# Optimization experiments

Hardware: AMD Instinct MI355X
Metric: run time of the kernel (lower is better)

Reference implementation:

```python
import jax, jax.numpy as jnp
import numpy as np

B, S, HID = 4, 1024, 1024
NH, HD = 16, 64  # num_heads, head_size
LEFT, RIGHT = 64, 8
NUM_POS = LEFT + RIGHT + 1  # 73


def setup_inputs() -> dict:
    key = jax.random.key(0)
    ks = jax.random.split(key, 11)
    s = 0.02
    return {
        "hidden_states": jax.random.normal(ks[0], (B, S, HID), jnp.float32),
        "Wq": jax.random.normal(ks[1], (HID, HID), jnp.float32) * s,
        "bq": jax.random.normal(ks[2], (HID,), jnp.float32) * s,
        "Wk": jax.random.normal(ks[3], (HID, HID), jnp.float32) * s,
        "bk": jax.random.normal(ks[4], (HID,), jnp.float32) * s,
        "Wv": jax.random.normal(ks[5], (HID, HID), jnp.float32) * s,
        "bv": jax.random.normal(ks[6], (HID,), jnp.float32) * s,
        "Wo": jax.random.normal(ks[7], (HID, HID), jnp.float32) * s,
        "bo": jax.random.normal(ks[8], (HID,), jnp.float32) * s,
        "dist_emb": jax.random.normal(ks[9], (NUM_POS, HD), jnp.float32) * s,
    }


def reference(hidden_states, Wq, bq, Wk, bk, Wv, bv, Wo, bo, dist_emb):
    inv_sqrt_d = 1.0 / np.sqrt(HD).astype(np.float32)
    # projections; nn.Linear: x @ W.T + b
    q = (hidden_states @ Wq.T + bq).reshape(B, S, NH, HD).transpose(0, 2, 1, 3)  # bhld
    k = (hidden_states @ Wk.T + bk).reshape(B, S, NH, HD).transpose(0, 2, 1, 3)
    v = (hidden_states @ Wv.T + bv).reshape(B, S, NH, HD).transpose(0, 2, 1, 3)

    scores = jnp.einsum("bhld,bhrd->bhlr", q, k) * inv_sqrt_d

    # relative_key bias
    pos_l = jnp.arange(S)[:, None]
    pos_r = jnp.arange(S)[None, :]
    dist = jnp.clip(pos_r - pos_l, -LEFT, RIGHT) + LEFT  # [S,S] in [0, NUM_POS)
    pos_emb = dist_emb[dist]  # [S,S,HD]
    rel = jnp.einsum("bhld,lrd->bhlr", q, pos_emb) * inv_sqrt_d
    scores = scores + rel

    probs = jax.nn.softmax(scores, axis=-1)  # dropout p=0 (eval)
    ctx = jnp.einsum("bhlr,bhrd->bhld", probs, v)
    ctx = ctx.transpose(0, 2, 1, 3).reshape(B, S, HID)
    out = ctx @ Wo.T + bo
    return (out, probs)
```

## Files before the change

### kernel.cpp

```cpp
#include <hip/hip_runtime.h>


using short8 = __attribute__((ext_vector_type(8))) short;
using f32x4  = __attribute__((ext_vector_type(4))) float;
using fl4    = __attribute__((ext_vector_type(4))) float;
using u16x4  = __attribute__((ext_vector_type(4))) unsigned short;

#define MFMA16(a, b, c) __builtin_amdgcn_mfma_f32_16x16x32_bf16((a), (b), (c), 0, 0, 0)

#define SCL2E 0.18033688011112042f

__device__ __forceinline__ float bf2f(unsigned short u) {
  union { unsigned int i; float f; } c;
  c.i = ((unsigned int)u) << 16;
  return c.f;
}
__device__ __forceinline__ unsigned short f2bf(float f) {
  union { float f; unsigned int i; } c;
  c.f = f;
  unsigned int x = c.i;
  return (unsigned short)((x + 0x7fffu + ((x >> 16) & 1u)) >> 16);
}
__device__ __forceinline__ float u2f(unsigned u) {
  union { unsigned i; float f; } c;
  c.i = u;
  return c.f;
}

__device__ __forceinline__ void gload_lds16(const void* g, void* l) {
  __builtin_amdgcn_global_load_lds(
      (const __attribute__((address_space(1))) void*)g,
      (__attribute__((address_space(3))) void*)l, 16, 0, 0);
}

__global__ void cvt_f32_bf16(const float* __restrict__ in,
                             unsigned short* __restrict__ out, int n4) {
  int i = blockIdx.x * blockDim.x + threadIdx.x;
  int stride = gridDim.x * blockDim.x;
  for (; i < n4; i += stride) {
    fl4 v = ((const fl4*)in)[i];
    u16x4 o;
    o[0] = f2bf(v[0]); o[1] = f2bf(v[1]); o[2] = f2bf(v[2]); o[3] = f2bf(v[3]);
    ((u16x4*)out)[i] = o;
  }
}

__global__ void cvt_w4(const float* __restrict__ w0, const float* __restrict__ w1,
                       const float* __restrict__ w2, const float* __restrict__ w3,
                       unsigned short* __restrict__ o0, unsigned short* __restrict__ o1,
                       unsigned short* __restrict__ o2, unsigned short* __restrict__ o3) {
  const int which = blockIdx.x >> 8;
  const float* in = which == 0 ? w0 : which == 1 ? w1 : which == 2 ? w2 : w3;
  unsigned short* out = which == 0 ? o0 : which == 1 ? o1 : which == 2 ? o2 : o3;
  int i = (blockIdx.x & 255) * 256 + threadIdx.x;
#pragma unroll
  for (int it = 0; it < 4; ++it, i += 65536) {
    fl4 v = ((const fl4*)in)[i];
    u16x4 o;
    o[0] = f2bf(v[0]); o[1] = f2bf(v[1]); o[2] = f2bf(v[2]); o[3] = f2bf(v[3]);
    ((u16x4*)out)[i] = o;
  }
}

__global__ void cvt_demb(const float* __restrict__ in,
                         unsigned short* __restrict__ out) {
  int i = blockIdx.x * blockDim.x + threadIdx.x;
  if (i < 80 * 64) out[i] = (i < 73 * 64) ? f2bf(in[i]) : (unsigned short)0;
}

__global__ __launch_bounds__(256)
void gemm_qkv3(const unsigned short* __restrict__ X,
               const unsigned short* __restrict__ Bq,
               const unsigned short* __restrict__ Bk,
               const unsigned short* __restrict__ Bv,
               const float* __restrict__ biq, const float* __restrict__ bik,
               const float* __restrict__ biv,
               unsigned short* __restrict__ Cq, unsigned short* __restrict__ Ck,
               unsigned short* __restrict__ Cvt) {
  __shared__ unsigned short lA[128 * 32];
  __shared__ unsigned short lB[128 * 32];
  const int i = blockIdx.x;
  const int wgid = (i & 7) * 96 + (i >> 3);
  const int r = wgid >> 8;
  const int id = wgid & 255;
  int bm, bn;
  const unsigned short *Aa, *Bb;
  if (r == 2) {
    bm = (id >> 5) * 128; bn = (id & 31) * 128;
    Aa = Bv; Bb = X;
  } else {
    bm = (id >> 3) * 128; bn = (id & 7) * 128;
    Aa = X; Bb = (r == 0) ? Bq : Bk;
  }
  const float* bias = (r == 0) ? biq : (r == 1) ? bik : biv;
  unsigned short* C = (r == 0) ? Cq : (r == 1) ? Ck : Cvt;
  const size_t cstride = (r == 2) ? 4096 : 1024;

  const int tid = threadIdx.x;
  const int wave = tid >> 6, lane = tid & 63;
  const int wm = wave >> 1, wn = wave & 1;

  f32x4 acc[4][4];
#pragma unroll
  for (int m = 0; m < 4; ++m)
#pragma unroll
    for (int n = 0; n < 4; ++n) acc[m][n] = (f32x4){0.f, 0.f, 0.f, 0.f};

  const int t0 = tid, t1 = tid + 256;
  const int ar0 = t0 >> 2, ak0 = (t0 & 3) * 8;
  const int ar1 = t1 >> 2, ak1 = (t1 & 3) * 8;
  const unsigned short* Ab = Aa + (size_t)bm * 1024;
  const unsigned short* Bbb = Bb + (size_t)bn * 1024;
  const int fr = lane & 15, fk = (lane >> 4) * 8;

  for (int kt = 0; kt < 1024; kt += 32) {
    gload_lds16(Ab + (size_t)ar0 * 1024 + kt + ak0, (void*)&lA[(wave * 64) * 8]);
    gload_lds16(Ab + (size_t)ar1 * 1024 + kt + ak1, (void*)&lA[2048 + (wave * 64) * 8]);
    gload_lds16(Bbb + (size_t)ar0 * 1024 + kt + ak0, (void*)&lB[(wave * 64) * 8]);
    gload_lds16(Bbb + (size_t)ar1 * 1024 + kt + ak1, (void*)&lB[2048 + (wave * 64) * 8]);
    __syncthreads();
    short8 af[4], bf[4];
#pragma unroll
    for (int m = 0; m < 4; ++m)
      af[m] = *(const short8*)&lA[(wm * 64 + m * 16 + fr) * 32 + fk];
#pragma unroll
    for (int n = 0; n < 4; ++n)
      bf[n] = *(const short8*)&lB[(wn * 64 + n * 16 + fr) * 32 + fk];
#pragma unroll
    for (int m = 0; m < 4; ++m)
#pragma unroll
      for (int n = 0; n < 4; ++n) acc[m][n] = MFMA16(af[m], bf[n], acc[m][n]);
    __syncthreads();
  }

  const int cr = (lane >> 4) * 4, cc = lane & 15;
#pragma unroll
  for (int m = 0; m < 4; ++m)
#pragma unroll
    for (int n = 0; n < 4; ++n) {
      const int col = bn + wn * 64 + n * 16 + cc;
#pragma unroll
      for (int g = 0; g < 4; ++g) {
        const int row = bm + wm * 64 + m * 16 + cr + g;
        const float bb = (r == 2) ? bias[row] : bias[col];
        C[(size_t)row * cstride + col] = f2bf(acc[m][n][g] + bb);
      }
    }
}

__global__ __launch_bounds__(256)
void gemm_nt_f32(const unsigned short* __restrict__ A,
                 const unsigned short* __restrict__ B,
                 const float* __restrict__ bias, float* __restrict__ Cp) {
  __shared__ unsigned short lA[128 * 32];
  __shared__ unsigned short lB[128 * 32];
  const int tid = threadIdx.x;
  const int wave = tid >> 6, lane = tid & 63;
  const int wm = wave >> 1, wn = wave & 1;
  const int bm = blockIdx.x * 128, bn = blockIdx.y * 128;

  f32x4 acc[4][4];
#pragma unroll
  for (int m = 0; m < 4; ++m)
#pragma unroll
    for (int n = 0; n < 4; ++n) acc[m][n] = (f32x4){0.f, 0.f, 0.f, 0.f};

  const int t0 = tid, t1 = tid + 256;
  const int ar0 = t0 >> 2, ak0 = (t0 & 3) * 8;
  const int ar1 = t1 >> 2, ak1 = (t1 & 3) * 8;
  const unsigned short* Ab = A + (size_t)bm * 1024;
  const unsigned short* Bb = B + (size_t)bn * 1024;
  const int fr = lane & 15, fk = (lane >> 4) * 8;

  for (int kt = 0; kt < 1024; kt += 32) {
    gload_lds16(Ab + (size_t)ar0 * 1024 + kt + ak0, (void*)&lA[(wave * 64) * 8]);
    gload_lds16(Ab + (size_t)ar1 * 1024 + kt + ak1, (void*)&lA[2048 + (wave * 64) * 8]);
    gload_lds16(Bb + (size_t)ar0 * 1024 + kt + ak0, (void*)&lB[(wave * 64) * 8]);
    gload_lds16(Bb + (size_t)ar1 * 1024 + kt + ak1, (void*)&lB[2048 + (wave * 64) * 8]);
    __syncthreads();
    short8 af[4], bf[4];
#pragma unroll
    for (int m = 0; m < 4; ++m)
      af[m] = *(const short8*)&lA[(wm * 64 + m * 16 + fr) * 32 + fk];
#pragma unroll
    for (int n = 0; n < 4; ++n)
      bf[n] = *(const short8*)&lB[(wn * 64 + n * 16 + fr) * 32 + fk];
#pragma unroll
    for (int m = 0; m < 4; ++m)
#pragma unroll
      for (int n = 0; n < 4; ++n) acc[m][n] = MFMA16(af[m], bf[n], acc[m][n]);
    __syncthreads();
  }

  const int cr = (lane >> 4) * 4, cc = lane & 15;
#pragma unroll
  for (int m = 0; m < 4; ++m)
#pragma unroll
    for (int n = 0; n < 4; ++n) {
      const int col = bn + wn * 64 + n * 16 + cc;
#pragma unroll
      for (int g = 0; g < 4; ++g) {
        const int row = bm + wm * 64 + m * 16 + cr + g;
        Cp[(size_t)row * 1024 + col] = acc[m][n][g] + bias[col];
      }
    }
}

__global__ __launch_bounds__(256, 2)
void attn_kernel(const unsigned short* __restrict__ q,
                 const unsigned short* __restrict__ k,
                 const unsigned short* __restrict__ vt,
                 const unsigned short* __restrict__ demb_bf,
                 float* __restrict__ probs,
                 unsigned short* __restrict__ ctx) {
  const int i = blockIdx.x;
  const int x = i & 7, s = i >> 3;
  const int bh = ((s >> 5) << 3) + x;
  const int qseg = s & 31;
  const int hd = bh & 15, b = bh >> 4;
  const int tid = threadIdx.x, w = tid >> 6, lane = tid & 63;
  const int lq = lane & 15, Qr = lane >> 4;
  const int qA = qseg * 32, qB = qA + 16;
  const int rowperm = ((lq >> 2) << 3) + (lq & 3);

  __shared__ unsigned short qdc[32][78];
  __shared__ float reds[4][32];
  __shared__ float red[4][4][32][16];

  const unsigned short* qpA =
      q + ((size_t)(b * 1024 + qA + lq)) * 1024 + hd * 64 + Qr * 8;
  short8 bqA0 = *(const short8*)qpA;
  short8 bqA1 = *(const short8*)(qpA + 32);
  const unsigned short* qpB = qpA + (size_t)16 * 1024;
  short8 bqB0 = *(const short8*)qpB;
  short8 bqB1 = *(const short8*)(qpB + 32);

  for (int pgq = w; pgq < 10; pgq += 4) {
    const int qblk = pgq >= 5;
    const int pg = qblk ? pgq - 5 : pgq;
    const unsigned short* dp = demb_bf + (size_t)(pg * 16 + lq) * 64 + Qr * 8;
    short8 a0 = *(const short8*)dp;
    short8 a1 = *(const short8*)(dp + 32);
    f32x4 c = (f32x4){0.f, 0.f, 0.f, 0.f};
    c = MFMA16(a0, qblk ? bqB0 : bqA0, c);
    c = MFMA16(a1, qblk ? bqB1 : bqA1, c);
#pragma unroll
    for (int g = 0; g < 4; ++g) {
      const int p = pg * 16 + Qr * 4 + g;
      if (p < 73) qdc[qblk * 16 + lq][p] = f2bf(c[g] * SCL2E);
    }
  }
  __syncthreads();

  const float qd0A = bf2f(qdc[lq][0]),       qd72A = bf2f(qdc[lq][72]);
  const float qd0B = bf2f(qdc[16 + lq][0]),  qd72B = bf2f(qdc[16 + lq][72]);

  float ssumA = 0.f, ssumB = 0.f;
  unsigned pafA[8][4], pafB[8][4];
  f32x4 oA0 = (f32x4){0.f, 0.f, 0.f, 0.f}, oA1 = oA0, oA2 = oA0, oA3 = oA0;
  f32x4 oB0 = oA0, oB1 = oA0, oB2 = oA0, oB3 = oA0;
  const unsigned short* kbase =
      k + ((size_t)(b * 1024 + w * 256 + rowperm)) * 1024 + hd * 64 + Qr * 8;
  const unsigned short* vb =
      vt + ((size_t)(hd * 64 + lq)) * 4096 + b * 1024 + w * 256 + Qr * 8;

#pragma unroll
  for (int t = 0; t < 8; ++t) {
    const unsigned short* kp = kbase + t * 32768;
    short8 ae0 = *(const short8*)kp;
    short8 ae1 = *(const short8*)(kp + 32);
    short8 ao0 = *(const short8*)(kp + 4096);
    short8 ao1 = *(const short8*)(kp + 4128);
    short8 v0 = *(const short8*)(vb + t * 32);
    short8 v1 = *(const short8*)(vb + (size_t)16 * 4096 + t * 32);
    short8 v2 = *(const short8*)(vb + (size_t)32 * 4096 + t * 32);
    short8 v3 = *(const short8*)(vb + (size_t)48 * 4096 + t * 32);

    f32x4 seA = (f32x4){0.f, 0.f, 0.f, 0.f}, soA = seA, seB = seA, soB = seA;
    seA = MFMA16(ae0, bqA0, seA); seA = MFMA16(ae1, bqA1, seA);
    soA = MFMA16(ao0, bqA0, soA); soA = MFMA16(ao1, bqA1, soA);
    seB = MFMA16(ae0, bqB0, seB); seB = MFMA16(ae1, bqB1, seB);
    soB = MFMA16(ao0, bqB0, soB); soB = MFMA16(ao1, bqB1, soB);

    const int tglob = w * 8 + t;
    {
      float pe[4], po[4];
      if (tglob * 32 + 31 < qA - 64) {
#pragma unroll
        for (int g = 0; g < 4; ++g) {
          pe[g] = exp2f(fmaf(seA[g], SCL2E, qd0A));
          po[g] = exp2f(fmaf(soA[g], SCL2E, qd0A));
        }
      } else if (tglob * 32 > qA + 23) {
#pragma unroll
        for (int g = 0; g < 4; ++g) {
          pe[g] = exp2f(fmaf(seA[g], SCL2E, qd72A));
          po[g] = exp2f(fmaf(soA[g], SCL2E, qd72A));
        }
      } else {
        const int c0 = tglob * 32 + Qr * 8 - (qA + lq);
#pragma unroll
        for (int g = 0; g < 4; ++g) {
          int d0 = c0 + g;     d0 = d0 < -64 ? -64 : (d0 > 8 ? 8 : d0);
          int d1 = c0 + 4 + g; d1 = d1 < -64 ? -64 : (d1 > 8 ? 8 : d1);
          pe[g] = exp2f(fmaf(seA[g], SCL2E, bf2f(qdc[lq][d0 + 64])));
          po[g] = exp2f(fmaf(soA[g], SCL2E, bf2f(qdc[lq][d1 + 64])));
        }
      }
#pragma unroll
      for (int g = 0; g < 4; ++g) ssumA += pe[g] + po[g];
      asm("v_cvt_pk_bf16_f32 %0, %1, %2" : "=v"(pafA[t][0]) : "v"(pe[0]), "v"(pe[1]));
      asm("v_cvt_pk_bf16_f32 %0, %1, %2" : "=v"(pafA[t][1]) : "v"(pe[2]), "v"(pe[3]));
      asm("v_cvt_pk_bf16_f32 %0, %1, %2" : "=v"(pafA[t][2]) : "v"(po[0]), "v"(po[1]));
      asm("v_cvt_pk_bf16_f32 %0, %1, %2" : "=v"(pafA[t][3]) : "v"(po[2]), "v"(po[3]));
      union { unsigned u[4]; short8 s8v; } uu;
      uu.u[0] = pafA[t][0]; uu.u[1] = pafA[t][1];
      uu.u[2] = pafA[t][2]; uu.u[3] = pafA[t][3];
      const short8 pa = uu.s8v;
      oA0 = MFMA16(pa, v0, oA0);
      oA1 = MFMA16(pa, v1, oA1);
      oA2 = MFMA16(pa, v2, oA2);
      oA3 = MFMA16(pa, v3, oA3);
    }
    {
      float pe[4], po[4];
      if (tglob * 32 + 31 < qB - 64) {
#pragma unroll
        for (int g = 0; g < 4; ++g) {
          pe[g] = exp2f(fmaf(seB[g], SCL2E, qd0B));
          po[g] = exp2f(fmaf(soB[g], SCL2E, qd0B));
        }
      } else if (tglob * 32 > qB + 23) {
#pragma unroll
        for (int g = 0; g < 4; ++g) {
          pe[g] = exp2f(fmaf(seB[g], SCL2E, qd72B));
          po[g] = exp2f(fmaf(soB[g], SCL2E, qd72B));
        }
      } else {
        const int c0 = tglob * 32 + Qr * 8 - (qB + lq);
#pragma unroll
        for (int g = 0; g < 4; ++g) {
          int d0 = c0 + g;     d0 = d0 < -64 ? -64 : (d0 > 8 ? 8 : d0);
          int d1 = c0 + 4 + g; d1 = d1 < -64 ? -64 : (d1 > 8 ? 8 : d1);
          pe[g] = exp2f(fmaf(seB[g], SCL2E, bf2f(qdc[16 + lq][d0 + 64])));
          po[g] = exp2f(fmaf(soB[g], SCL2E, bf2f(qdc[16 + lq][d1 + 64])));
        }
      }
#pragma unroll
      for (int g = 0; g < 4; ++g) ssumB += pe[g] + po[g];
      asm("v_cvt_pk_bf16_f32 %0, %1, %2" : "=v"(pafB[t][0]) : "v"(pe[0]), "v"(pe[1]));
      asm("v_cvt_pk_bf16_f32 %0, %1, %2" : "=v"(pafB[t][1]) : "v"(pe[2]), "v"(pe[3]));
      asm("v_cvt_pk_bf16_f32 %0, %1, %2" : "=v"(pafB[t][2]) : "v"(po[0]), "v"(po[1]));
      asm("v_cvt_pk_bf16_f32 %0, %1, %2" : "=v"(pafB[t][3]) : "v"(po[2]), "v"(po[3]));
      union { unsigned u[4]; short8 s8v; } uu;
      uu.u[0] = pafB[t][0]; uu.u[1] = pafB[t][1];
      uu.u[2] = pafB[t][2]; uu.u[3] = pafB[t][3];
      const short8 pa = uu.s8v;
      oB0 = MFMA16(pa, v0, oB0);
      oB1 = MFMA16(pa, v1, oB1);
      oB2 = MFMA16(pa, v2, oB2);
      oB3 = MFMA16(pa, v3, oB3);
    }
  }
  ssumA += __shfl_xor(ssumA, 16, 64);
  ssumA += __shfl_xor(ssumA, 32, 64);
  ssumB += __shfl_xor(ssumB, 16, 64);
  ssumB += __shfl_xor(ssumB, 32, 64);
  if (lane < 16) {
    reds[w][lane] = ssumA;
    reds[w][16 + lane] = ssumB;
  }
#pragma unroll
  for (int g = 0; g < 4; ++g) {
    red[w][0][Qr * 4 + g][lq] = oA0[g];
    red[w][1][Qr * 4 + g][lq] = oA1[g];
    red[w][2][Qr * 4 + g][lq] = oA2[g];
    red[w][3][Qr * 4 + g][lq] = oA3[g];
    red[w][0][16 + Qr * 4 + g][lq] = oB0[g];
    red[w][1][16 + Qr * 4 + g][lq] = oB1[g];
    red[w][2][16 + Qr * 4 + g][lq] = oB2[g];
    red[w][3][16 + Qr * 4 + g][lq] = oB3[g];
  }
  __syncthreads();

  const float invA =
      1.0f / (reds[0][lq] + reds[1][lq] + reds[2][lq] + reds[3][lq]);
  const float invB = 1.0f / (reds[0][16 + lq] + reds[1][16 + lq] +
                             reds[2][16 + lq] + reds[3][16 + lq]);
  float* prowA = probs + ((size_t)bh * 1024 + qA + lq) * 1024 + w * 256 + Qr * 8;
  float* prowB = prowA + (size_t)16 * 1024;
#pragma unroll
  for (int t = 0; t < 8; ++t) {
    f32x4 p0, p1;
    p0[0] = u2f(pafA[t][0] << 16) * invA;
    p0[1] = u2f(pafA[t][0] & 0xffff0000u) * invA;
    p0[2] = u2f(pafA[t][1] << 16) * invA;
    p0[3] = u2f(pafA[t][1] & 0xffff0000u) * invA;
    p1[0] = u2f(pafA[t][2] << 16) * invA;
    p1[1] = u2f(pafA[t][2] & 0xffff0000u) * invA;
    p1[2] = u2f(pafA[t][3] << 16) * invA;
    p1[3] = u2f(pafA[t][3] & 0xffff0000u) * invA;
    *(f32x4*)&prowA[t * 32] = p0;
    *(f32x4*)&prowA[t * 32 + 4] = p1;
    f32x4 q0, q1;
    q0[0] = u2f(pafB[t][0] << 16) * invB;
    q0[1] = u2f(pafB[t][0] & 0xffff0000u) * invB;
    q0[2] = u2f(pafB[t][1] << 16) * invB;
    q0[3] = u2f(pafB[t][1] & 0xffff0000u) * invB;
    q1[0] = u2f(pafB[t][2] << 16) * invB;
    q1[1] = u2f(pafB[t][2] & 0xffff0000u) * invB;
    q1[2] = u2f(pafB[t][3] << 16) * invB;
    q1[3] = u2f(pafB[t][3] & 0xffff0000u) * invB;
    *(f32x4*)&prowB[t * 32] = q0;
    *(f32x4*)&prowB[t * 32 + 4] = q1;
  }

  {
    const int qrow = tid >> 3;
    const int d0 = (tid & 7) * 8;
    const float invq = 1.0f / (reds[0][qrow] + reds[1][qrow] +
                               reds[2][qrow] + reds[3][qrow]);
    u16x4 cv0, cv1;
#pragma unroll
    for (int j = 0; j < 8; ++j) {
      const int d = d0 + j;
      const int db = d >> 4, dd = d & 15;
      float sum = red[0][db][qrow][dd] + red[1][db][qrow][dd] +
                  red[2][db][qrow][dd] + red[3][db][qrow][dd];
      if (j < 4) cv0[j] = f2bf(sum * invq);
      else       cv1[j - 4] = f2bf(sum * invq);
    }
    unsigned short* cb =
        ctx + ((size_t)(b * 1024 + qA + qrow)) * 1024 + hd * 64 + d0;
    *(u16x4*)cb = cv0;
    *(u16x4*)(cb + 4) = cv1;
  }
}

extern "C" void kernel_launch(void* const* d_in, const int* in_sizes, int n_in,
                              void* d_out, int out_size, void* d_ws, size_t ws_size,
                              hipStream_t stream) {
  const float* hs = (const float*)d_in[0];
  const float* Wq = (const float*)d_in[1];
  const float* bq = (const float*)d_in[2];
  const float* Wk = (const float*)d_in[3];
  const float* bk = (const float*)d_in[4];
  const float* Wv = (const float*)d_in[5];
  const float* bv = (const float*)d_in[6];
  const float* Wo = (const float*)d_in[7];
  const float* bo = (const float*)d_in[8];
  const float* de = (const float*)d_in[9];

  float* out = (float*)d_out;
  float* probs = out + (size_t)4 * 1024 * 1024;

  char* ws = (char*)d_ws;
  unsigned short* Xb  = (unsigned short*)(ws);
  unsigned short* Wqb = (unsigned short*)(ws + ((size_t)8 << 20));
  unsigned short* Wkb = (unsigned short*)(ws + ((size_t)10 << 20));
  unsigned short* Wvb = (unsigned short*)(ws + ((size_t)12 << 20));
  unsigned short* Wob = (unsigned short*)(ws + ((size_t)14 << 20));
  unsigned short* Qb  = (unsigned short*)(ws + ((size_t)16 << 20));
  unsigned short* Kb  = (unsigned short*)(ws + ((size_t)24 << 20));
  unsigned short* Vt  = (unsigned short*)(ws + ((size_t)32 << 20));
  unsigned short* Db  = Wqb;
  unsigned short* Cx  = Xb;

  cvt_f32_bf16<<<dim3(1024), dim3(256), 0, stream>>>(hs, Xb, (4 * 1024 * 1024) / 4);
  cvt_w4<<<dim3(1024), dim3(256), 0, stream>>>(Wq, Wk, Wv, Wo, Wqb, Wkb, Wvb, Wob);

  gemm_qkv3<<<dim3(768), dim3(256), 0, stream>>>(Xb, Wqb, Wkb, Wvb, bq, bk, bv,
                                                 Qb, Kb, Vt);
  cvt_demb<<<dim3(20), dim3(256), 0, stream>>>(de, Db);

  attn_kernel<<<dim3(2048), dim3(256), 0, stream>>>(Qb, Kb, Vt, Db, probs, Cx);

  gemm_nt_f32<<<dim3(32, 8), dim3(256), 0, stream>>>(Cx, Wob, bo, out);
}
```

Baseline: 192.5 us.

## Store Q, K, V in MFMA-fragment-tiled per-head layouts for contiguous attention loads

The QKV projection epilogue now writes Q, K and V into per-(batch,head) blocks laid out to match the MFMA operand fragments, with 512-element sub-tiles of 16 rows by 32 elements. The attention kernel then reads each short8 fragment from contiguous addresses instead of strided rows spanning the full hidden dimension. This targets scattered global loads in the attention inner loop. In exchange, the GEMM epilogue does scattered 2-byte stores with more index arithmetic, which may slow the projection kernel.

```diff
diff --git a/kernel.cpp b/kernel.cpp
--- a/kernel.cpp
+++ b/kernel.cpp
@@ -76,7 +76,7 @@
                const float* __restrict__ biq, const float* __restrict__ bik,
                const float* __restrict__ biv,
                unsigned short* __restrict__ Cq, unsigned short* __restrict__ Ck,
-               unsigned short* __restrict__ Cvt) {
+               unsigned short* __restrict__ Cv) {
   __shared__ unsigned short lA[128 * 32];
   __shared__ unsigned short lB[128 * 32];
   const int i = blockIdx.x;
@@ -93,8 +93,6 @@
     Aa = X; Bb = (r == 0) ? Bq : Bk;
   }
   const float* bias = (r == 0) ? biq : (r == 1) ? bik : biv;
-  unsigned short* C = (r == 0) ? Cq : (r == 1) ? Ck : Cvt;
-  const size_t cstride = (r == 2) ? 4096 : 1024;
 
   const int tid = threadIdx.x;
   const int wave = tid >> 6, lane = tid & 63;
@@ -142,8 +140,35 @@
 #pragma unroll
       for (int g = 0; g < 4; ++g) {
         const int row = bm + wm * 64 + m * 16 + cr + g;
-        const float bb = (r == 2) ? bias[row] : bias[col];
-        C[(size_t)row * cstride + col] = f2bf(acc[m][n][g] + bb);
+        if (r == 2) {
+          const float v = acc[m][n][g] + bias[row];
+          const int head = row >> 6, d = row & 63;
+          const int b2 = col >> 10, sl = col & 1023, kk = sl & 31;
+          size_t idx = ((size_t)((b2 << 4) + head) << 16) +
+                       (size_t)(((sl >> 5) * 4 + (d >> 4)) * 512) +
+                       (d & 15) * 32 + ((kk >> 3) * 8) + (kk & 7);
+          Cv[idx] = f2bf(v);
+        } else {
+          const float v = acc[m][n][g] + bias[col];
+          const int head = col >> 6, d = col & 63;
+          const int b2 = row >> 10, sl = row & 1023;
+          const int dc = d >> 3;
+          const size_t hb = (size_t)((b2 << 4) + head) << 16;
+          if (r == 0) {
+            size_t idx = hb +
+                         (size_t)((((sl >> 4) * 2 + (dc >> 2)) * 16 + (sl & 15)) * 32) +
+                         (dc & 3) * 8 + (d & 7);
+            Cq[idx] = f2bf(v);
+          } else {
+            const int kt2 = sl >> 5;
+            const int p = ((sl >> 3) & 3) * 4 + (sl & 3);
+            const int half = (sl >> 2) & 1;
+            size_t idx = hb +
+                         (size_t)((((kt2 * 2 + half) * 2 + (dc >> 2)) * 512)) +
+                         p * 32 + (dc & 3) * 8 + (d & 7);
+            Ck[idx] = f2bf(v);
+          }
+        }
       }
     }
 }
@@ -221,19 +246,19 @@
   const int tid = threadIdx.x, w = tid >> 6, lane = tid & 63;
   const int lq = lane & 15, Qr = lane >> 4;
   const int qA = qseg * 32, qB = qA + 16;
-  const int rowperm = ((lq >> 2) << 3) + (lq & 3);
 
   __shared__ unsigned short qdc[32][78];
   __shared__ float reds[4][32];
   __shared__ float red[4][4][32][16];
 
-  const unsigned short* qpA =
-      q + ((size_t)(b * 1024 + qA + lq)) * 1024 + hd * 64 + Qr * 8;
-  short8 bqA0 = *(const short8*)qpA;
-  short8 bqA1 = *(const short8*)(qpA + 32);
-  const unsigned short* qpB = qpA + (size_t)16 * 1024;
-  short8 bqB0 = *(const short8*)qpB;
-  short8 bqB1 = *(const short8*)(qpB + 32);
+  const size_t hb = (size_t)((b << 4) + hd) << 16;
+  const int lo16 = lq * 32 + Qr * 8;
+
+  const unsigned short* qh = q + hb + (size_t)(qseg * 4) * 512;
+  short8 bqA0 = *(const short8*)(qh + lo16);
+  short8 bqA1 = *(const short8*)(qh + 512 + lo16);
+  short8 bqB0 = *(const short8*)(qh + 1024 + lo16);
+  short8 bqB1 = *(const short8*)(qh + 1536 + lo16);
 
   for (int pgq = w; pgq < 10; pgq += 4) {
     const int qblk = pgq >= 5;
@@ -259,22 +284,22 @@
   unsigned pafA[8][4], pafB[8][4];
   f32x4 oA0 = (f32x4){0.f, 0.f, 0.f, 0.f}, oA1 = oA0, oA2 = oA0, oA3 = oA0;
   f32x4 oB0 = oA0, oB1 = oA0, oB2 = oA0, oB3 = oA0;
-  const unsigned short* kbase =
-      k + ((size_t)(b * 1024 + w * 256 + rowperm)) * 1024 + hd * 64 + Qr * 8;
-  const unsigned short* vb =
-      vt + ((size_t)(hd * 64 + lq)) * 4096 + b * 1024 + w * 256 + Qr * 8;
+
+  const unsigned short* kh = k + hb + (size_t)(w * 8) * 2048 + lo16;
+  const unsigned short* vh = vt + hb + (size_t)(w * 8) * 2048 + lo16;
 
 #pragma unroll
   for (int t = 0; t < 8; ++t) {
-    const unsigned short* kp = kbase + t * 32768;
+    const unsigned short* kp = kh + t * 2048;
     short8 ae0 = *(const short8*)kp;
-    short8 ae1 = *(const short8*)(kp + 32);
-    short8 ao0 = *(const short8*)(kp + 4096);
-    short8 ao1 = *(const short8*)(kp + 4128);
-    short8 v0 = *(const short8*)(vb + t * 32);
-    short8 v1 = *(const short8*)(vb + (size_t)16 * 4096 + t * 32);
-    short8 v2 = *(const short8*)(vb + (size_t)32 * 4096 + t * 32);
-    short8 v3 = *(const short8*)(vb + (size_t)48 * 4096 + t * 32);
+    short8 ae1 = *(const short8*)(kp + 512);
+    short8 ao0 = *(const short8*)(kp + 1024);
+    short8 ao1 = *(const short8*)(kp + 1536);
+    const unsigned short* vp = vh + t * 2048;
+    short8 v0 = *(const short8*)vp;
+    short8 v1 = *(const short8*)(vp + 512);
+    short8 v2 = *(const short8*)(vp + 1024);
+    short8 v3 = *(const short8*)(vp + 1536);
 
     f32x4 seA = (f32x4){0.f, 0.f, 0.f, 0.f}, soA = seA, seB = seA, soB = seA;
     seA = MFMA16(ae0, bqA0, seA); seA = MFMA16(ae1, bqA1, seA);
```

Result: faster. 176.0 us (-8.5%).
